# Kernel optimization log

Hardware: AMD Instinct MI355X
Metric: run time of the kernel (lower is better)

Reference implementation:

```python
import jax, jax.numpy as jnp
import numpy as np

N, B, D_IN, D_OUT, E = 1024, 128, 64, 64, 16


def setup_inputs() -> dict:
    key = jax.random.key(0)
    k1, k2, k3, k4 = jax.random.split(key, 4)
    x = jax.random.normal(k1, (B, N, D_IN), dtype=jnp.float32)
    node_embeddings = jax.random.normal(k2, (N, E), dtype=jnp.float32)
    weights_pool = jax.random.normal(k3, (E, D_IN, D_OUT), dtype=jnp.float32)
    bias_pool = jax.random.normal(k4, (E, D_OUT), dtype=jnp.float32)
    return {"x": x, "node_embeddings": node_embeddings,
            "weights_pool": weights_pool, "bias_pool": bias_pool}


def reference(x, node_embeddings, weights_pool, bias_pool):
    # Adaptive adjacency: softmax over rows of relu(E E^T), shape [N, N]
    scores = jax.nn.relu(node_embeddings @ node_embeddings.T)
    supports = jax.nn.softmax(scores, axis=1)
    # Per-node weights [N, D_IN, D_OUT] and bias [N, D_OUT]
    weights = jnp.einsum('nd,dio->nio', node_embeddings, weights_pool)
    bias = node_embeddings @ bias_pool  # [N, D_OUT]
    # Graph aggregation: [B, N, D_IN]
    x_g = jnp.einsum('nm,bmc->bnc', supports, x)
    # Per-node linear transform + bias: [B, N, D_OUT]
    x_gconv = jnp.einsum('bni,nio->bno', x_g, weights) + bias
    return x_gconv
```

## Files before the change

kernel.cpp:

```cpp
#include <hip/hip_runtime.h>

#define N_NODES 1024
#define BATCH   128
#define E_DIM   16


typedef __attribute__((ext_vector_type(8))) short bf16x8;
typedef __attribute__((ext_vector_type(4))) float f32x4;
typedef __attribute__((ext_vector_type(16))) float f32x16;

__device__ __forceinline__ unsigned short f2bf(float f) {
    union { float f; unsigned int u; } v; v.f = f;
    unsigned int u = v.u;
    u += 0x7FFFu + ((u >> 16) & 1u);
    return (unsigned short)(u >> 16);
}

__device__ __forceinline__ void gload_lds16(const void* g, void* l) {
    __builtin_amdgcn_global_load_lds(
        (const __attribute__((address_space(1))) unsigned int*)g,
        (__attribute__((address_space(3))) unsigned int*)l, 16, 0, 0);
}

__global__ __launch_bounds__(256) void k_xt(const float* __restrict__ x,
                                            unsigned short* __restrict__ xbt) {
    const int bid = blockIdx.x;
    const int t = threadIdx.x;
    const int b = bid >> 4, kt64 = bid & 15;
    unsigned short* dstp = xbt + (long)(b >> 1) * 131072 + kt64 * 8192
                         + (b & 1) * 512;
#pragma unroll
    for (int h = 0; h < 2; ++h) {
        const int g = h * 256 + t;
        const int kblk = g >> 6, c = g & 63;
        const float* s = x + ((long)b * 1024 + kt64 * 64 + kblk * 8) * 64 + c;
        bf16x8 r;
#pragma unroll
        for (int e = 0; e < 8; ++e) r[e] = (short)f2bf(s[e * 64]);
        *(bf16x8*)(dstp + kblk * 1024 + c * 8) = r;
    }
}

__global__ __launch_bounds__(256) void k_wsup(const float* __restrict__ emb,
                                              const float* __restrict__ wpool,
                                              const float* __restrict__ bpool,
                                              unsigned short* __restrict__ sup,
                                              unsigned short* __restrict__ Wt,
                                              float* __restrict__ bias) {
    __shared__ float sm[132];
    const int bid = blockIdx.x;
    const int t = threadIdx.x;

    if (bid < 256) {
        float (*en4)[E_DIM] = (float(*)[E_DIM])sm;
        const int n0 = bid * 4;
        if (t < 64) en4[t >> 4][t & 15] = emb[(n0 + (t >> 4)) * E_DIM + (t & 15)];
        __syncthreads();
        const int o = t & 63;
#pragma unroll
        for (int p = 0; p < 2; ++p) {
            const int kblk = p * 4 + (t >> 6);
            float w[4][8];
#pragma unroll
            for (int nn = 0; nn < 4; ++nn)
#pragma unroll
                for (int e = 0; e < 8; ++e) w[nn][e] = 0.f;
            for (int ed = 0; ed < E_DIM; ++ed) {
                float v[8];
#pragma unroll
                for (int e = 0; e < 8; ++e)
                    v[e] = wpool[ed * 4096 + (kblk * 8 + e) * 64 + o];
#pragma unroll
                for (int nn = 0; nn < 4; ++nn)
#pragma unroll
                    for (int e = 0; e < 8; ++e)
                        w[nn][e] = fmaf(en4[nn][ed], v[e], w[nn][e]);
            }
#pragma unroll
            for (int nn = 0; nn < 4; ++nn) {
                bf16x8 r;
#pragma unroll
                for (int e = 0; e < 8; ++e) r[e] = (short)f2bf(w[nn][e]);
                *(bf16x8*)(Wt + (long)(n0 + nn) * 4096 + kblk * 512 + o * 8) = r;
            }
        }
        {
            const int nn = t >> 6, oo = t & 63;
            float s = 0.f;
#pragma unroll
            for (int e = 0; e < E_DIM; ++e) s = fmaf(en4[nn][e], bpool[e * 64 + oo], s);
            bias[(n0 + nn) * 64 + oo] = s;
        }
    } else {
        float* en  = sm;
        float* red = sm + 128;
        const int n = bid - 256;
        if (t < E_DIM) en[t] = emb[n * E_DIM + t];
        __syncthreads();
        float sc[4];
        float mx = -1e30f;
#pragma unroll
        for (int r = 0; r < 4; ++r) {
            const float* em = &emb[(r * 256 + t) * E_DIM];
            float s = 0.f;
#pragma unroll
            for (int e = 0; e < E_DIM; ++e) s = fmaf(en[e], em[e], s);
            s = fmaxf(s, 0.f);
            sc[r] = s;
            mx = fmaxf(mx, s);
        }
#pragma unroll
        for (int o = 32; o > 0; o >>= 1) mx = fmaxf(mx, __shfl_xor(mx, o));
        if ((t & 63) == 0) red[t >> 6] = mx;
        __syncthreads();
        mx = fmaxf(fmaxf(red[0], red[1]), fmaxf(red[2], red[3]));
        float sum = 0.f;
#pragma unroll
        for (int r = 0; r < 4; ++r) { sc[r] = __expf(sc[r] - mx); sum += sc[r]; }
#pragma unroll
        for (int o = 32; o > 0; o >>= 1) sum += __shfl_xor(sum, o);
        __syncthreads();
        if ((t & 63) == 0) red[t >> 6] = sum;
        __syncthreads();
        sum = red[0] + red[1] + red[2] + red[3];
        const float inv = 1.f / sum;
#pragma unroll
        for (int r = 0; r < 4; ++r) {
            const int m = r * 256 + t;
            const int off = (n >> 7) * 131072 + (m >> 6) * 8192 + ((m >> 3) & 7) * 1024
                          + (n & 127) * 8 + (m & 7);
            sup[off] = f2bf(sc[r] * inv);
        }
    }
}

__global__ __launch_bounds__(256, 2) void k_agg(const unsigned short* __restrict__ S,
                                                const unsigned short* __restrict__ Bt,
                                                unsigned short* __restrict__ xg) {
    __shared__ __align__(16) char lds[65536];
    const int t = threadIdx.x;
    const int lane = t & 63, wid = t >> 6;

    const int hw   = blockIdx.x + 8 * blockIdx.y;
    const int work = (hw & 7) * 64 + (hw >> 3);
    const int n0 = (work & 7) * 128, j0 = (work >> 3) * 128;
    const int wr = wid >> 1, wc = wid & 1;

    f32x16 acc[2][2];
#pragma unroll
    for (int m = 0; m < 2; ++m)
#pragma unroll
        for (int n = 0; n < 2; ++n)
#pragma unroll
            for (int r = 0; r < 16; ++r) acc[m][n][r] = 0.f;

    const unsigned short* pA = S  + (n0 >> 7) * 131072 + lane * 8;
    const unsigned short* pB = Bt + (j0 >> 7) * 131072 + lane * 8;
    const unsigned short* sp[4];
    int doff[4];
#pragma unroll
    for (int i = 0; i < 4; ++i) {
        const int c = wid * 4 + i;
        if (c < 8) { sp[i] = pA + c * 512;       doff[i] = c * 1024; }
        else       { sp[i] = pB + (c - 8) * 512; doff[i] = 8192 + (c - 8) * 1024; }
    }
#define STAGE(kt) do {                                                   \
        char* buf_ = lds + ((kt) & 3) * 16384;                           \
        const int ko_ = (kt) * 4096;                                     \
        gload_lds16(sp[0] + ko_, buf_ + doff[0]);                        \
        gload_lds16(sp[1] + ko_, buf_ + doff[1]);                        \
        gload_lds16(sp[2] + ko_, buf_ + doff[2]);                        \
        gload_lds16(sp[3] + ko_, buf_ + doff[3]);                        \
    } while (0)

    int aoff[2], boff[2];
#pragma unroll
    for (int m = 0; m < 2; ++m)
        aoff[m] = (lane >> 5) * 2048 + (wr * 64 + m * 32 + (lane & 31)) * 16;
#pragma unroll
    for (int n = 0; n < 2; ++n)
        boff[n] = 8192 + (lane >> 5) * 2048 + (wc * 64 + n * 32 + (lane & 31)) * 16;

    STAGE(0); STAGE(1);
    for (int kt = 0; kt < 32; ++kt) {
        if (kt < 31) asm volatile("s_waitcnt vmcnt(4)" ::: "memory");
        else         asm volatile("s_waitcnt vmcnt(0)" ::: "memory");
        __builtin_amdgcn_s_barrier();
        asm volatile("" ::: "memory");
        __builtin_amdgcn_sched_barrier(0);
        if (kt + 2 < 32) STAGE(kt + 2);
        const char* cur = lds + (kt & 3) * 16384;
        __builtin_amdgcn_s_setprio(1);
#pragma unroll
        for (int s = 0; s < 2; ++s) {
            bf16x8 a[2], b[2];
#pragma unroll
            for (int m = 0; m < 2; ++m) a[m] = *(const bf16x8*)(cur + s * 4096 + aoff[m]);
#pragma unroll
            for (int n = 0; n < 2; ++n) b[n] = *(const bf16x8*)(cur + s * 4096 + boff[n]);
#pragma unroll
            for (int m = 0; m < 2; ++m)
#pragma unroll
                for (int n = 0; n < 2; ++n)
                    acc[m][n] = __builtin_amdgcn_mfma_f32_32x32x16_bf16(a[m], b[n], acc[m][n], 0, 0, 0);
        }
        __builtin_amdgcn_s_setprio(0);
        asm volatile("" ::: "memory");
        __builtin_amdgcn_sched_barrier(0);
    }
#undef STAGE
    __syncthreads();

    char* lb = lds;
#pragma unroll
    for (int m = 0; m < 2; ++m) {
#pragma unroll
        for (int n = 0; n < 2; ++n) {
            const int col  = wc * 64 + n * 32 + (lane & 31);
            const int rowb = wr * 64 + m * 32 + 4 * (lane >> 5);
#pragma unroll
            for (int r = 0; r < 16; ++r) {
                const int row = rowb + (r & 3) + 8 * (r >> 2);
                *(unsigned short*)(lb + row * 256 + ((col * 2) ^ ((row & 7) << 4))) =
                    f2bf(acc[m][n][r]);
            }
        }
    }
    __syncthreads();
    const int b0 = j0 >> 6;
#pragma unroll
    for (int i = 0; i < 8; ++i) {
        const int idx = i * 256 + t;
        const int row = idx >> 4, cc = idx & 15;
        bf16x8 v = *(const bf16x8*)(lb + row * 256 + ((cc * 16) ^ ((row & 7) << 4)));
        const int b = b0 + (cc >> 3);
        const long dst = (long)(n0 + row) * 8192 + b * 64 + ((cc & 7) ^ (b & 7)) * 8;
        *(bf16x8*)(xg + dst) = v;
    }
}

__global__ __launch_bounds__(256) void k_out(const unsigned short* __restrict__ xg,
                                             const unsigned short* __restrict__ Wt,
                                             const float* __restrict__ bias,
                                             float* __restrict__ out) {
    __shared__ __align__(16) char lds[49152];
    const int t = threadIdx.x, lane = t & 63, wid = t >> 6;
    const int nb = blockIdx.x * 2;
#pragma unroll
    for (int i = 0; i < 12; ++i) {
        const int c = wid * 12 + i;
        if (c < 32) {
            const int nn = c >> 4, k = c & 15;
            gload_lds16(xg + (long)(nb + nn) * 8192 + k * 512 + lane * 8,
                        lds + nn * 16384 + k * 1024);
        } else {
            const int cc = c - 32, nn = cc >> 3, k = cc & 7;
            gload_lds16(Wt + (long)(nb + nn) * 4096 + k * 512 + lane * 8,
                        lds + 32768 + nn * 8192 + k * 1024);
        }
    }
    __syncthreads();

    const int node = nb + (wid >> 1);
    const int bh   = wid & 1;
    const char* xl = lds + (wid >> 1) * 16384;
    const char* wlp = lds + 32768 + (wid >> 1) * 8192;

    f32x4 acc[4][4];
#pragma unroll
    for (int m = 0; m < 4; ++m)
#pragma unroll
        for (int n = 0; n < 4; ++n) acc[m][n] = f32x4{0.f, 0.f, 0.f, 0.f};

#pragma unroll
    for (int s = 0; s < 2; ++s) {
        const int kb = s * 4 + (lane >> 4);
        bf16x8 a[4], b[4];
#pragma unroll
        for (int m = 0; m < 4; ++m) {
            const int brow = bh * 64 + m * 16 + (lane & 15);
            a[m] = *(const bf16x8*)(xl + brow * 128 + ((kb ^ (lane & 7)) << 4));
        }
#pragma unroll
        for (int n = 0; n < 4; ++n)
            b[n] = *(const bf16x8*)(wlp + kb * 1024 + (n * 16 + (lane & 15)) * 16);
#pragma unroll
        for (int m = 0; m < 4; ++m)
#pragma unroll
            for (int n = 0; n < 4; ++n)
                acc[m][n] = __builtin_amdgcn_mfma_f32_16x16x32_bf16(a[m], b[n], acc[m][n], 0, 0, 0);
    }

#pragma unroll
    for (int n = 0; n < 4; ++n) {
        const int o = n * 16 + (lane & 15);
        const float bv = bias[node * 64 + o];
#pragma unroll
        for (int m = 0; m < 4; ++m) {
            const int b0 = bh * 64 + m * 16 + (lane >> 4) * 4;
#pragma unroll
            for (int r = 0; r < 4; ++r)
                out[(long)(b0 + r) * 65536 + node * 64 + o] = acc[m][n][r] + bv;
        }
    }
}

extern "C" void kernel_launch(void* const* d_in, const int* in_sizes, int n_in,
                              void* d_out, int out_size, void* d_ws, size_t ws_size,
                              hipStream_t stream) {
    const float* x     = (const float*)d_in[0];
    const float* emb   = (const float*)d_in[1];
    const float* wpool = (const float*)d_in[2];
    const float* bpool = (const float*)d_in[3];
    float* out = (float*)d_out;

    char* ws = (char*)d_ws;
    unsigned short* sup  = (unsigned short*)(ws);
    unsigned short* xbt  = (unsigned short*)(ws + (2u  << 20));
    unsigned short* Wt   = (unsigned short*)(ws + (18u << 20));
    float*          bias = (float*)         (ws + (26u << 20));
    unsigned short* xg   = (unsigned short*)(ws + (27u << 20));
    (void)in_sizes; (void)n_in; (void)out_size; (void)ws_size;

    k_xt<<<dim3(2048), dim3(256), 0, stream>>>(x, xbt);
    k_wsup<<<dim3(1280), dim3(256), 0, stream>>>(emb, wpool, bpool, sup, Wt, bias);
    k_agg<<<dim3(8, 64), dim3(256), 0, stream>>>(sup, xbt, xg);
    k_out<<<dim3(512), dim3(256), 0, stream>>>(xg, Wt, bias, out);
}
```

Measured before the change: 56.99 us.

## Load MFMA fragments directly from global memory in k_agg, bypassing LDS staging

Replaces the LDS-staged, barrier-synchronised 4-buffer pipeline in the aggregation GEMM with direct per-lane global loads of bf16 fragments into registers, software-pipelined three steps ahead across a fully unrolled 64-step K loop. This removes the per-iteration barriers and LDS round trips, and halves the LDS allocation since shared memory is now only used for the epilogue. In exchange, each wave loads its own A/B fragments, so data shared between waves is no longer reused through LDS. This adds global/L2 traffic and register pressure, and the full unroll grows code size.

```diff
diff --git a/kernel.cpp b/kernel.cpp
--- a/kernel.cpp
+++ b/kernel.cpp
@@ -137,7 +137,7 @@
 __global__ __launch_bounds__(256, 2) void k_agg(const unsigned short* __restrict__ S,
                                                 const unsigned short* __restrict__ Bt,
                                                 unsigned short* __restrict__ xg) {
-    __shared__ __align__(16) char lds[65536];
+    __shared__ __align__(16) char lds[32768];
     const int t = threadIdx.x;
     const int lane = t & 63, wid = t >> 6;
 
@@ -154,62 +154,34 @@
 #pragma unroll
             for (int r = 0; r < 16; ++r) acc[m][n][r] = 0.f;
 
-    const unsigned short* pA = S  + (n0 >> 7) * 131072 + lane * 8;
-    const unsigned short* pB = Bt + (j0 >> 7) * 131072 + lane * 8;
-    const unsigned short* sp[4];
-    int doff[4];
-#pragma unroll
-    for (int i = 0; i < 4; ++i) {
-        const int c = wid * 4 + i;
-        if (c < 8) { sp[i] = pA + c * 512;       doff[i] = c * 1024; }
-        else       { sp[i] = pB + (c - 8) * 512; doff[i] = 8192 + (c - 8) * 1024; }
-    }
-#define STAGE(kt) do {                                                   \
-        char* buf_ = lds + ((kt) & 3) * 16384;                           \
-        const int ko_ = (kt) * 4096;                                     \
-        gload_lds16(sp[0] + ko_, buf_ + doff[0]);                        \
-        gload_lds16(sp[1] + ko_, buf_ + doff[1]);                        \
-        gload_lds16(sp[2] + ko_, buf_ + doff[2]);                        \
-        gload_lds16(sp[3] + ko_, buf_ + doff[3]);                        \
+    const int lh = lane >> 5, lr = lane & 31;
+    const unsigned short* baseA = S  + (n0 >> 7) * 131072 + (wr * 64 + lr) * 8;
+    const unsigned short* baseB = Bt + (j0 >> 7) * 131072 + (wc * 64 + lr) * 8;
+
+    bf16x8 fa[3][2], fb[3][2];
+#define KOFF(s_) (((s_) >> 2) * 8192 + ((2 * (s_) + lh) & 7) * 1024)
+#define LOADF(ph, s_) do {                                           \
+        const int ko_ = KOFF(s_);                                    \
+        fa[ph][0] = *(const bf16x8*)(baseA + ko_);                   \
+        fa[ph][1] = *(const bf16x8*)(baseA + ko_ + 256);             \
+        fb[ph][0] = *(const bf16x8*)(baseB + ko_);                   \
+        fb[ph][1] = *(const bf16x8*)(baseB + ko_ + 256);             \
     } while (0)
 
-    int aoff[2], boff[2];
-#pragma unroll
-    for (int m = 0; m < 2; ++m)
-        aoff[m] = (lane >> 5) * 2048 + (wr * 64 + m * 32 + (lane & 31)) * 16;
-#pragma unroll
-    for (int n = 0; n < 2; ++n)
-        boff[n] = 8192 + (lane >> 5) * 2048 + (wc * 64 + n * 32 + (lane & 31)) * 16;
-
-    STAGE(0); STAGE(1);
-    for (int kt = 0; kt < 32; ++kt) {
-        if (kt < 31) asm volatile("s_waitcnt vmcnt(4)" ::: "memory");
-        else         asm volatile("s_waitcnt vmcnt(0)" ::: "memory");
-        __builtin_amdgcn_s_barrier();
-        asm volatile("" ::: "memory");
-        __builtin_amdgcn_sched_barrier(0);
-        if (kt + 2 < 32) STAGE(kt + 2);
-        const char* cur = lds + (kt & 3) * 16384;
-        __builtin_amdgcn_s_setprio(1);
-#pragma unroll
-        for (int s = 0; s < 2; ++s) {
-            bf16x8 a[2], b[2];
-#pragma unroll
-            for (int m = 0; m < 2; ++m) a[m] = *(const bf16x8*)(cur + s * 4096 + aoff[m]);
-#pragma unroll
-            for (int n = 0; n < 2; ++n) b[n] = *(const bf16x8*)(cur + s * 4096 + boff[n]);
-#pragma unroll
-            for (int m = 0; m < 2; ++m)
-#pragma unroll
-                for (int n = 0; n < 2; ++n)
-                    acc[m][n] = __builtin_amdgcn_mfma_f32_32x32x16_bf16(a[m], b[n], acc[m][n], 0, 0, 0);
-        }
-        __builtin_amdgcn_s_setprio(0);
-        asm volatile("" ::: "memory");
-        __builtin_amdgcn_sched_barrier(0);
-    }
-#undef STAGE
-    __syncthreads();
+    LOADF(0, 0); LOADF(1, 1); LOADF(2, 2);
+#pragma unroll
+    for (int s = 0; s < 64; ++s) {
+        const int ph = s % 3;
+#pragma unroll
+        for (int m = 0; m < 2; ++m)
+#pragma unroll
+            for (int n = 0; n < 2; ++n)
+                acc[m][n] = __builtin_amdgcn_mfma_f32_32x32x16_bf16(
+                    fa[ph][m], fb[ph][n], acc[m][n], 0, 0, 0);
+        if (s + 3 < 64) LOADF(ph, s + 3);
+    }
+#undef LOADF
+#undef KOFF
 
     char* lb = lds;
 #pragma unroll
```

Result: slower. 62.58 us (+9.8%).
